# Performance work log

Hardware: AMD Instinct MI355X
Metric: run time of the kernel (lower is better)

Reference implementation:

```python
import jax, jax.numpy as jnp
import numpy as np

HEAD_SIZE = 64
INPUT_SIZE = 1024
B, T = 8, 2048


def setup_inputs() -> dict:
    key = jax.random.key(0)
    kx, kq, kk, kv = jax.random.split(key, 4)
    x = jax.random.normal(kx, (B, T, INPUT_SIZE), dtype=jnp.float32)
    s = 1.0 / np.sqrt(INPUT_SIZE)
    Wq = jax.random.uniform(kq, (INPUT_SIZE, HEAD_SIZE), minval=-s, maxval=s, dtype=jnp.float32)
    Wk = jax.random.uniform(kk, (INPUT_SIZE, HEAD_SIZE), minval=-s, maxval=s, dtype=jnp.float32)
    Wv = jax.random.uniform(kv, (INPUT_SIZE, HEAD_SIZE), minval=-s, maxval=s, dtype=jnp.float32)
    return {"x": x, "Wq": Wq, "Wk": Wk, "Wv": Wv}


def reference(x, Wq, Wk, Wv):
    # Faithful to the torch module: scores = K @ Q^T (note: keys times queries^T),
    # causal mask on upper triangle of that matrix, softmax over last axis,
    # dropout treated as identity (eval), then scores @ V.
    q = jnp.einsum('bti,ih->bth', x, Wq)  # [B,T,H]
    k = jnp.einsum('bti,ih->bth', x, Wk)
    v = jnp.einsum('bti,ih->bth', x, Wv)
    scale = HEAD_SIZE ** -0.5
    scores = jnp.einsum('bth,bsh->bts', k, q) * scale  # [B,T,T] = K Q^T
    Tlen = x.shape[1]
    causal = jnp.tril(jnp.ones((Tlen, Tlen), dtype=bool))
    scores = jnp.where(causal, scores, -jnp.inf)
    w = jax.nn.softmax(scores, axis=-1)
    out = jnp.einsum('bts,bsh->bth', w, v)  # [B,T,H]
    return out
```

## Files before the change

kernel.cpp:

```cpp
#include <hip/hip_runtime.h>

typedef __bf16 bf16_t;
typedef bf16_t bf16x8 __attribute__((ext_vector_type(8)));
typedef float f32x4 __attribute__((ext_vector_type(4)));

#define NB 8
#define TT 2048
#define DIN 1024
#define HH 64
#define MM (NB * TT)

#define CHUNK 4
#define BPB 144
#define NSLOT (NB * BPB)

__device__ __forceinline__ unsigned short f2bf(float f) {
    unsigned int u = __float_as_uint(f);
    u += 0x7fffu + ((u >> 16) & 1u);
    return (unsigned short)(u >> 16);
}

__device__ __forceinline__ void async16(void* l, const void* g) {
    __builtin_amdgcn_global_load_lds(
        (const __attribute__((address_space(1))) unsigned int*)g,
        (__attribute__((address_space(3))) unsigned int*)l, 16, 0, 0);
}

__device__ __forceinline__ int block_detect_f32(const unsigned int* __restrict__ xw,
                                                int tid, int* sflag) {
    if (tid < 64) {
        unsigned int u = xw[tid];
        unsigned int e = (u >> 7) & 0xFFu;
        unsigned long long m = __ballot(e >= 100u && e <= 150u);
        if (tid == 0) *sflag = (__popcll(m) < 48) ? 1 : 0;
    }
    __syncthreads();
    return *sflag;
}

__global__ __launch_bounds__(256) void transpose_w_kernel(
    const void* __restrict__ Wq, const void* __restrict__ Wk,
    const void* __restrict__ Wv, const unsigned int* __restrict__ xw,
    unsigned short* __restrict__ Wt) {
    __shared__ int sflag;
    __shared__ unsigned short ts[64][68];
    const int tid = threadIdx.x;
    const int isf32 = block_detect_f32(xw, tid, &sflag);
    const int w = blockIdx.x >> 4, kt = blockIdx.x & 15;
    const void* W = (w == 0) ? Wq : (w == 1) ? Wk : Wv;
    const int kk = tid >> 4, nn = (tid & 15) * 4;
#pragma unroll
    for (int j = 0; j < 4; ++j) {
        int k = kk + j * 16;
        if (isf32) {
            float4 f = *(const float4*)((const float*)W + (size_t)(kt * 64 + k) * 64 + nn);
            ts[k][nn + 0] = f2bf(f.x); ts[k][nn + 1] = f2bf(f.y);
            ts[k][nn + 2] = f2bf(f.z); ts[k][nn + 3] = f2bf(f.w);
        } else {
            *(uint2*)&ts[k][nn] =
                *(const uint2*)((const unsigned short*)W + (size_t)(kt * 64 + k) * 64 + nn);
        }
    }
    __syncthreads();
    const int n = tid >> 2, k0 = (tid & 3) * 16;
    unsigned short tmp[16];
#pragma unroll
    for (int j = 0; j < 16; ++j) tmp[j] = ts[k0 + j][n];
    unsigned short* dst = Wt + (size_t)(w * 64 + n) * 1024 + kt * 64 + k0;
    *(uint4*)(dst + 0) = *(uint4*)&tmp[0];
    *(uint4*)(dst + 8) = *(uint4*)&tmp[8];
}

#define PN 48

__global__ __launch_bounds__(256, 2) void proj_kernel(
    const void* __restrict__ xraw, const unsigned short* __restrict__ Wt,
    unsigned short* __restrict__ qbuf, unsigned short* __restrict__ kbuf,
    unsigned short* __restrict__ vtbuf) {
    __shared__ int sflag;
    __shared__ __align__(16) unsigned char xsb[64 * 128];
    __shared__ __align__(16) unsigned char wldsb[PN * 128];

    const int tid = threadIdx.x;
    const int isf32 = block_detect_f32((const unsigned int*)xraw, tid, &sflag);
    const int m0 = blockIdx.x * 64;
    const int nh = blockIdx.y;
    const int wave = tid >> 6, lane = tid & 63, quad = lane >> 4, l15 = lane & 15;

    const float* xf = (const float*)xraw;
    const unsigned short* xb = (const unsigned short*)xraw;
    const unsigned char* wg = (const unsigned char*)Wt;

    const unsigned char* wsrc[2];
    unsigned int wdst[2];
    int nw = 0;
#pragma unroll
    for (int j = 0; j < 2; ++j) {
        int c = tid + 256 * j;
        if (c < PN * 8) {
            int R = c >> 3, cc = c & 7;
            int g = cc ^ (R & 7);
            wsrc[nw] = wg + (size_t)(nh * PN + R) * 2048 + g * 16;
            wdst[nw] = c * 16;
            ++nw;
        }
    }

    const int xr = tid >> 2, xc = (tid & 3) * 16;
    const unsigned int xb0 = (unsigned int)(((xc >> 3) ^ (xr & 7)) * 16);
    const unsigned int xb1 = (unsigned int)((((xc >> 3) + 1) ^ (xr & 7)) * 16);
    float4 px[4];
    uint4  pxb[2];
    auto ldx = [&](int k0) {
        if (isf32) {
            const float* g = xf + (size_t)(m0 + xr) * DIN + k0 + xc;
#pragma unroll
            for (int j = 0; j < 4; ++j) px[j] = *(const float4*)(g + j * 4);
        } else {
            const unsigned short* g = xb + (size_t)(m0 + xr) * DIN + k0 + xc;
            pxb[0] = *(const uint4*)(g + 0);
            pxb[1] = *(const uint4*)(g + 8);
        }
    };

    f32x4 acc[3];
#pragma unroll
    for (int ct = 0; ct < 3; ++ct) acc[ct] = (f32x4){0.f, 0.f, 0.f, 0.f};

    ldx(0);
    size_t woff = 0;
    for (int it = 0; it < 16; ++it) {
        __syncthreads();
        {
            unsigned char* xrow = xsb + xr * 128;
            if (isf32) {
                unsigned short t[16];
#pragma unroll
                for (int j = 0; j < 4; ++j) {
                    t[j * 4 + 0] = f2bf(px[j].x); t[j * 4 + 1] = f2bf(px[j].y);
                    t[j * 4 + 2] = f2bf(px[j].z); t[j * 4 + 3] = f2bf(px[j].w);
                }
                *(uint4*)(xrow + xb0) = *(uint4*)&t[0];
                *(uint4*)(xrow + xb1) = *(uint4*)&t[8];
            } else {
                *(uint4*)(xrow + xb0) = pxb[0];
                *(uint4*)(xrow + xb1) = pxb[1];
            }
        }
        for (int j = 0; j < nw; ++j) async16(&wldsb[wdst[j]], wsrc[j] + woff);
        woff += 128;
        __syncthreads();

        if (it < 15) ldx((it + 1) * 64);

#pragma unroll
        for (int ks = 0; ks < 2; ++ks) {
            const int arow = wave * 16 + l15;
            bf16x8 a = *(const bf16x8*)
                (xsb + arow * 128 + (((ks * 4 + quad) ^ (arow & 7)) * 16));
            bf16x8 b[3];
#pragma unroll
            for (int ct = 0; ct < 3; ++ct) {
                const int ri = ct * 16 + l15;
                b[ct] = *(const bf16x8*)
                    (wldsb + ri * 128 + (((ks * 4 + quad) ^ (ri & 7)) * 16));
            }
#pragma unroll
            for (int ct = 0; ct < 3; ++ct)
                acc[ct] = __builtin_amdgcn_mfma_f32_16x16x32_bf16(
                    a, b[ct], acc[ct], 0, 0, 0);
        }
    }

#pragma unroll
    for (int ct = 0; ct < 3; ++ct) {
        int n = nh * PN + ct * 16 + l15;
        int wsel = n >> 6, nn = n & 63;
#pragma unroll
        for (int reg = 0; reg < 4; ++reg) {
            int m = m0 + wave * 16 + quad * 4 + reg;
            unsigned short bv = f2bf(acc[ct][reg]);
            if (wsel == 0)      qbuf[(size_t)m * HH + nn] = bv;
            else if (wsel == 1) kbuf[(size_t)m * HH + nn] = bv;
            else {
                int bb = m >> 11, t = m & 2047;
                vtbuf[((size_t)bb * HH + nn) * TT + t] = bv;
            }
        }
    }
}

__global__ __launch_bounds__(256, 4) void attn_kernel(
    const unsigned short* __restrict__ rowbuf,
    const unsigned short* __restrict__ colbuf,
    const unsigned short* __restrict__ vtbuf,
    float* __restrict__ O_part,
    float* __restrict__ l_part) {

    __shared__ __align__(16) unsigned char Qb[64 * 128];
    __shared__ __align__(16) unsigned char Kb[64 * 128];
    __shared__ __align__(16) unsigned char Vb[64 * 128];
    __shared__ __align__(16) unsigned char Pb[4][16 * 128];

    const int tid  = threadIdx.x;
    const int bid  = blockIdx.x;
    const int b    = bid & 7;
    const int bx   = bid >> 3;
    int rt = 0, ch = 0;
    {
        int a = 0;
        for (int r = 0; r < 32; ++r) {
            int nc = (r + CHUNK) >> 2;
            if (bx < a + nc) { rt = r; ch = bx - a; break; }
            a += nc;
        }
    }
    const int nct = min(CHUNK, rt + 1 - ch * CHUNK);
    const int t0 = rt * 64;
    const int slot = b * BPB + bx;

    const int wave = tid >> 6, lane = tid & 63, quad = lane >> 4, l15 = lane & 15;
    const int sr = tid >> 2, sc = (tid & 3) * 16;
    const unsigned int sb0 = (unsigned int)(((sc >> 3) ^ (sr & 7)) * 16);
    const unsigned int sb1 = (unsigned int)((((sc >> 3) + 1) ^ (sr & 7)) * 16);

    {
        const uint4* g = (const uint4*)(rowbuf + ((size_t)b * TT + t0 + sr) * HH + sc);
        unsigned char* qrow = Qb + sr * 128;
        *(uint4*)(qrow + sb0) = g[0];
        *(uint4*)(qrow + sb1) = g[1];
    }

    f32x4 o[4];
#pragma unroll
    for (int c = 0; c < 4; ++c) o[c] = (f32x4){0.f, 0.f, 0.f, 0.f};
    float ls[4] = {0.f, 0.f, 0.f, 0.f};

    const float SCL2 = 0.125f * 1.4426950408889634f;

    uint4 pk0, pk1, pv0, pv1;
    auto loadKV = [&](int i) {
        const int s0 = (ch * CHUNK + i) * 64;
        const uint4* gk = (const uint4*)(colbuf + ((size_t)b * TT + s0 + sr) * HH + sc);
        pk0 = gk[0]; pk1 = gk[1];
        const uint4* gv = (const uint4*)(vtbuf + ((size_t)b * HH + sr) * TT + s0 + sc);
        pv0 = gv[0]; pv1 = gv[1];
    };
    loadKV(0);

    for (int i = 0; i < nct; ++i) {
        const int stc = ch * CHUNK + i;
        const int s0 = stc * 64;
        {
            unsigned char* krow = Kb + sr * 128;
            unsigned char* vrow = Vb + sr * 128;
            *(uint4*)(krow + sb0) = pk0;
            *(uint4*)(krow + sb1) = pk1;
            *(uint4*)(vrow + sb0) = pv0;
            *(uint4*)(vrow + sb1) = pv1;
        }
        __syncthreads();

        f32x4 scf[4];
#pragma unroll
        for (int c = 0; c < 4; ++c) scf[c] = (f32x4){0.f, 0.f, 0.f, 0.f};
        __builtin_amdgcn_s_setprio(1);
#pragma unroll
        for (int ks = 0; ks < 2; ++ks) {
            const int arow = wave * 16 + l15;
            bf16x8 a = *(const bf16x8*)
                (Qb + arow * 128 + (((ks * 4 + quad) ^ (arow & 7)) * 16));
#pragma unroll
            for (int c = 0; c < 4; ++c) {
                const int ri = c * 16 + l15;
                bf16x8 bb = *(const bf16x8*)
                    (Kb + ri * 128 + (((ks * 4 + quad) ^ (ri & 7)) * 16));
                scf[c] = __builtin_amdgcn_mfma_f32_16x16x32_bf16(a, bb, scf[c], 0, 0, 0);
            }
        }
        __builtin_amdgcn_s_setprio(0);

        if (i + 1 < nct) loadKV(i + 1);

        const bool diag = (stc == rt);
#pragma unroll
        for (int r = 0; r < 4; ++r) {
            const int tg = t0 + wave * 16 + quad * 4 + r;
            const int rr = quad * 4 + r;
            unsigned char* prow = Pb[wave] + rr * 128;
#pragma unroll
            for (int c = 0; c < 4; ++c) {
                float arg = fmaf(scf[c][r], SCL2, -30.f);
                if (diag && (s0 + c * 16 + l15) > tg) arg = -200.f;
                float p = __builtin_amdgcn_exp2f(arg);
                const int cc2 = c * 16 + l15;
                *(unsigned short*)(prow + (((cc2 >> 3) ^ (rr & 7)) * 16)
                                        + (cc2 & 7) * 2) = f2bf(p);
                ls[r] += p;
            }
        }
        __builtin_amdgcn_s_setprio(1);
#pragma unroll
        for (int ks = 0; ks < 2; ++ks) {
            bf16x8 ap = *(const bf16x8*)
                (Pb[wave] + l15 * 128 + (((ks * 4 + quad) ^ (l15 & 7)) * 16));
#pragma unroll
            for (int c = 0; c < 4; ++c) {
                const int ri = c * 16 + l15;
                bf16x8 bv = *(const bf16x8*)
                    (Vb + ri * 128 + (((ks * 4 + quad) ^ (ri & 7)) * 16));
                o[c] = __builtin_amdgcn_mfma_f32_16x16x32_bf16(ap, bv, o[c], 0, 0, 0);
            }
        }
        __builtin_amdgcn_s_setprio(0);
        __syncthreads();
    }

#pragma unroll
    for (int r = 0; r < 4; ++r) {
#pragma unroll
        for (int off = 1; off < 16; off <<= 1) ls[r] += __shfl_xor(ls[r], off);
    }
    if (l15 == 0) {
#pragma unroll
        for (int r = 0; r < 4; ++r)
            l_part[(size_t)slot * 64 + wave * 16 + quad * 4 + r] = ls[r];
    }
#pragma unroll
    for (int c = 0; c < 4; ++c)
#pragma unroll
        for (int r = 0; r < 4; ++r)
            O_part[(size_t)slot * 4096 + (wave * 16 + quad * 4 + r) * 64 + c * 16 + l15] = o[c][r];
}

__global__ __launch_bounds__(256) void combine_kernel(
    const float* __restrict__ O_part, const float* __restrict__ l_part,
    const unsigned int* __restrict__ xw, void* __restrict__ outraw) {
    __shared__ int sflag;
    const int tid = threadIdx.x;
    const int isf32 = block_detect_f32(xw, tid, &sflag);
    const int bid = blockIdx.x;
    const int b = bid & 7;
    const int rg = bid >> 3;
    const int rt = rg >> 2, qr = rg & 3;
    const int nch = (rt + CHUNK) >> 2;
    int off = 0;
    for (int r = 0; r < rt; ++r) off += (r + CHUNK) >> 2;
    const int slot0 = b * BPB + off;

    const int row = qr * 16 + (tid >> 4);
    const int cb = (tid & 15) * 4;
    f32x4 a = (f32x4){0.f, 0.f, 0.f, 0.f};
    float l = 0.f;
    for (int j = 0; j < nch; ++j) {
        a += *(const f32x4*)(O_part + (size_t)(slot0 + j) * 4096 + row * 64 + cb);
        l += l_part[(size_t)(slot0 + j) * 64 + row];
    }
    const float inv = 1.f / l;
    const size_t base = ((size_t)b * TT + rt * 64 + row) * HH + cb;
    if (isf32) {
        f32x4 v = a * inv;
        *(f32x4*)((float*)outraw + base) = v;
    } else {
        unsigned short h[4];
#pragma unroll
        for (int e = 0; e < 4; ++e) h[e] = f2bf(a[e] * inv);
        *(uint2*)((unsigned short*)outraw + base) = *(uint2*)&h[0];
    }
}

extern "C" void kernel_launch(void* const* d_in, const int* in_sizes, int n_in,
                              void* d_out, int out_size, void* d_ws, size_t ws_size,
                              hipStream_t stream) {
    const void* x  = d_in[0];
    const void* Wq = d_in[1];
    const void* Wk = d_in[2];
    const void* Wv = d_in[3];
    unsigned short* ws = (unsigned short*)d_ws;

    unsigned short* qbuf  = ws;
    unsigned short* kbuf  = ws + (size_t)MM * HH;
    unsigned short* vtbuf = ws + (size_t)2 * MM * HH;
    unsigned short* wtbuf = ws + (size_t)3 * MM * HH;
    float* O_part = (float*)(ws + (size_t)3 * MM * HH + 3 * 65536);
    float* l_part = O_part + (size_t)NSLOT * 4096;

    hipLaunchKernelGGL(transpose_w_kernel, dim3(48), dim3(256), 0, stream,
                       Wq, Wk, Wv, (const unsigned int*)x, wtbuf);
    hipLaunchKernelGGL(proj_kernel, dim3(256, 4), dim3(256), 0, stream,
                       x, wtbuf, qbuf, kbuf, vtbuf);
    hipLaunchKernelGGL(attn_kernel, dim3(NSLOT), dim3(256), 0, stream,
                       kbuf, qbuf, vtbuf, O_part, l_part);
    hipLaunchKernelGGL(combine_kernel, dim3(1024), dim3(256), 0, stream,
                       O_part, l_part, (const unsigned int*)x, d_out);
}
```

Baseline: 143.5 us.

## Load projection operands directly from global into MFMA registers, dropping LDS staging

The projection kernel no longer stages x and W tiles through shared memory with barriers. Each lane now loads its MFMA fragments straight from global memory into registers, double-buffered across k-iterations, and the occupancy hint rises from 2 to 4 blocks per CU. This removes the LDS writes and reads, the swizzling and the __syncthreads per iteration. In exchange each wave re-reads the W fragments from global/L2 with less coalesced 16-byte-per-lane accesses, and fp32-to-bf16 conversion now uses the compiler cast instead of the manual rounding helper.

```diff
diff --git a/kernel.cpp b/kernel.cpp
--- a/kernel.cpp
+++ b/kernel.cpp
@@ -18,12 +18,6 @@
     unsigned int u = __float_as_uint(f);
     u += 0x7fffu + ((u >> 16) & 1u);
     return (unsigned short)(u >> 16);
-}
-
-__device__ __forceinline__ void async16(void* l, const void* g) {
-    __builtin_amdgcn_global_load_lds(
-        (const __attribute__((address_space(1))) unsigned int*)g,
-        (__attribute__((address_space(3))) unsigned int*)l, 16, 0, 0);
 }
 
 __device__ __forceinline__ int block_detect_f32(const unsigned int* __restrict__ xw,
@@ -73,102 +67,103 @@
 
 #define PN 48
 
-__global__ __launch_bounds__(256, 2) void proj_kernel(
+__global__ __launch_bounds__(256, 4) void proj_kernel(
     const void* __restrict__ xraw, const unsigned short* __restrict__ Wt,
     unsigned short* __restrict__ qbuf, unsigned short* __restrict__ kbuf,
     unsigned short* __restrict__ vtbuf) {
     __shared__ int sflag;
-    __shared__ __align__(16) unsigned char xsb[64 * 128];
-    __shared__ __align__(16) unsigned char wldsb[PN * 128];
-
     const int tid = threadIdx.x;
     const int isf32 = block_detect_f32((const unsigned int*)xraw, tid, &sflag);
     const int m0 = blockIdx.x * 64;
     const int nh = blockIdx.y;
     const int wave = tid >> 6, lane = tid & 63, quad = lane >> 4, l15 = lane & 15;
 
-    const float* xf = (const float*)xraw;
-    const unsigned short* xb = (const unsigned short*)xraw;
+    const int arow = m0 + wave * 16 + l15;
+    const float* xrowf = (const float*)xraw + (size_t)arow * DIN + quad * 8;
+    const unsigned short* xrowb = (const unsigned short*)xraw + (size_t)arow * DIN + quad * 8;
+
     const unsigned char* wg = (const unsigned char*)Wt;
-
-    const unsigned char* wsrc[2];
-    unsigned int wdst[2];
-    int nw = 0;
-#pragma unroll
-    for (int j = 0; j < 2; ++j) {
-        int c = tid + 256 * j;
-        if (c < PN * 8) {
-            int R = c >> 3, cc = c & 7;
-            int g = cc ^ (R & 7);
-            wsrc[nw] = wg + (size_t)(nh * PN + R) * 2048 + g * 16;
-            wdst[nw] = c * 16;
-            ++nw;
-        }
-    }
-
-    const int xr = tid >> 2, xc = (tid & 3) * 16;
-    const unsigned int xb0 = (unsigned int)(((xc >> 3) ^ (xr & 7)) * 16);
-    const unsigned int xb1 = (unsigned int)((((xc >> 3) + 1) ^ (xr & 7)) * 16);
-    float4 px[4];
-    uint4  pxb[2];
-    auto ldx = [&](int k0) {
-        if (isf32) {
-            const float* g = xf + (size_t)(m0 + xr) * DIN + k0 + xc;
-#pragma unroll
-            for (int j = 0; j < 4; ++j) px[j] = *(const float4*)(g + j * 4);
-        } else {
-            const unsigned short* g = xb + (size_t)(m0 + xr) * DIN + k0 + xc;
-            pxb[0] = *(const uint4*)(g + 0);
-            pxb[1] = *(const uint4*)(g + 8);
+    const unsigned char* wp0 = wg + (size_t)(nh * PN +  0 + l15) * 2048 + quad * 16;
+    const unsigned char* wp1 = wg + (size_t)(nh * PN + 16 + l15) * 2048 + quad * 16;
+    const unsigned char* wp2 = wg + (size_t)(nh * PN + 32 + l15) * 2048 + quad * 16;
+
+    f32x4 acc[3];
+#pragma unroll
+    for (int ct = 0; ct < 3; ++ct) acc[ct] = (f32x4){0.f, 0.f, 0.f, 0.f};
+
+    auto loadw = [&](int it, uint4 (&w)[6]) {
+        const size_t o = (size_t)it * 128;
+#pragma unroll
+        for (int ks = 0; ks < 2; ++ks) {
+            w[0 * 2 + ks] = *(const uint4*)(wp0 + o + ks * 64);
+            w[1 * 2 + ks] = *(const uint4*)(wp1 + o + ks * 64);
+            w[2 * 2 + ks] = *(const uint4*)(wp2 + o + ks * 64);
         }
     };
-
-    f32x4 acc[3];
-#pragma unroll
-    for (int ct = 0; ct < 3; ++ct) acc[ct] = (f32x4){0.f, 0.f, 0.f, 0.f};
-
-    ldx(0);
-    size_t woff = 0;
-    for (int it = 0; it < 16; ++it) {
-        __syncthreads();
-        {
-            unsigned char* xrow = xsb + xr * 128;
-            if (isf32) {
-                unsigned short t[16];
-#pragma unroll
-                for (int j = 0; j < 4; ++j) {
-                    t[j * 4 + 0] = f2bf(px[j].x); t[j * 4 + 1] = f2bf(px[j].y);
-                    t[j * 4 + 2] = f2bf(px[j].z); t[j * 4 + 3] = f2bf(px[j].w);
-                }
-                *(uint4*)(xrow + xb0) = *(uint4*)&t[0];
-                *(uint4*)(xrow + xb1) = *(uint4*)&t[8];
-            } else {
-                *(uint4*)(xrow + xb0) = pxb[0];
-                *(uint4*)(xrow + xb1) = pxb[1];
-            }
-        }
-        for (int j = 0; j < nw; ++j) async16(&wldsb[wdst[j]], wsrc[j] + woff);
-        woff += 128;
-        __syncthreads();
-
-        if (it < 15) ldx((it + 1) * 64);
-
-#pragma unroll
-        for (int ks = 0; ks < 2; ++ks) {
-            const int arow = wave * 16 + l15;
-            bf16x8 a = *(const bf16x8*)
-                (xsb + arow * 128 + (((ks * 4 + quad) ^ (arow & 7)) * 16));
-            bf16x8 b[3];
-#pragma unroll
-            for (int ct = 0; ct < 3; ++ct) {
-                const int ri = ct * 16 + l15;
-                b[ct] = *(const bf16x8*)
-                    (wldsb + ri * 128 + (((ks * 4 + quad) ^ (ri & 7)) * 16));
-            }
-#pragma unroll
-            for (int ct = 0; ct < 3; ++ct)
-                acc[ct] = __builtin_amdgcn_mfma_f32_16x16x32_bf16(
-                    a, b[ct], acc[ct], 0, 0, 0);
+    auto wfrag = [](const uint4& u) -> bf16x8 {
+        union { uint4 u; bf16x8 b; } c; c.u = u; return c.b;
+    };
+
+    if (isf32) {
+        auto loadx = [&](int it, float4 (&x)[4]) {
+            const float* p = xrowf + it * 64;
+#pragma unroll
+            for (int ks = 0; ks < 2; ++ks) {
+                x[ks * 2 + 0] = *(const float4*)(p + ks * 32);
+                x[ks * 2 + 1] = *(const float4*)(p + ks * 32 + 4);
+            }
+        };
+        auto mk = [](const float4& f0, const float4& f1) -> bf16x8 {
+            bf16x8 a;
+            a[0] = (bf16_t)f0.x; a[1] = (bf16_t)f0.y;
+            a[2] = (bf16_t)f0.z; a[3] = (bf16_t)f0.w;
+            a[4] = (bf16_t)f1.x; a[5] = (bf16_t)f1.y;
+            a[6] = (bf16_t)f1.z; a[7] = (bf16_t)f1.w;
+            return a;
+        };
+        auto compute = [&](float4 (&x)[4], uint4 (&w)[6]) {
+#pragma unroll
+            for (int ks = 0; ks < 2; ++ks) {
+                bf16x8 a = mk(x[ks * 2], x[ks * 2 + 1]);
+#pragma unroll
+                for (int ct = 0; ct < 3; ++ct)
+                    acc[ct] = __builtin_amdgcn_mfma_f32_16x16x32_bf16(
+                        a, wfrag(w[ct * 2 + ks]), acc[ct], 0, 0, 0);
+            }
+        };
+        float4 xA[4], xB[4];
+        uint4  wA[6], wB[6];
+        loadx(0, xA); loadw(0, wA);
+        for (int it = 0; it < 16; it += 2) {
+            loadx(it + 1, xB); loadw(it + 1, wB);
+            compute(xA, wA);
+            if (it + 2 < 16) { loadx(it + 2, xA); loadw(it + 2, wA); }
+            compute(xB, wB);
+        }
+    } else {
+        auto loadx = [&](int it, uint4 (&x)[2]) {
+            const unsigned short* p = xrowb + it * 64;
+            x[0] = *(const uint4*)(p + 0 * 32);
+            x[1] = *(const uint4*)(p + 1 * 32);
+        };
+        auto compute = [&](uint4 (&x)[2], uint4 (&w)[6]) {
+#pragma unroll
+            for (int ks = 0; ks < 2; ++ks) {
+                bf16x8 a = wfrag(x[ks]);
+#pragma unroll
+                for (int ct = 0; ct < 3; ++ct)
+                    acc[ct] = __builtin_amdgcn_mfma_f32_16x16x32_bf16(
+                        a, wfrag(w[ct * 2 + ks]), acc[ct], 0, 0, 0);
+            }
+        };
+        uint4 xA[2], xB[2];
+        uint4 wA[6], wB[6];
+        loadx(0, xA); loadw(0, wA);
+        for (int it = 0; it < 16; it += 2) {
+            loadx(it + 1, xB); loadw(it + 1, wB);
+            compute(xA, wA);
+            if (it + 2 < 16) { loadx(it + 2, xA); loadw(it + 2, wA); }
+            compute(xB, wB);
         }
     }
 
```

Result: slower. 186.7 us (+30.1%).

## Halve projection barriers with double-wide W stage; keep Q fragments in registers

Applied to the files above, without the earlier changes.

The projection kernel now loads two 64-wide K slices of W per barrier pair into a doubled LDS buffer and runs two compute steps between syncs. This halves the number of __syncthreads per block, at the cost of extra LDS use. Separately, the attention kernel drops the Q shared-memory tile and loads each wave's Q MFMA operands straight from global memory into registers. That removes LDS traffic and LDS footprint, in exchange for more registers and an uncoalesced Q load.

```diff
diff --git a/kernel.cpp b/kernel.cpp
--- a/kernel.cpp
+++ b/kernel.cpp
@@ -79,7 +79,7 @@
     unsigned short* __restrict__ vtbuf) {
     __shared__ int sflag;
     __shared__ __align__(16) unsigned char xsb[64 * 128];
-    __shared__ __align__(16) unsigned char wldsb[PN * 128];
+    __shared__ __align__(16) unsigned char wldsb[2 * PN * 128];
 
     const int tid = threadIdx.x;
     const int isf32 = block_detect_f32((const unsigned int*)xraw, tid, &sflag);
@@ -91,19 +91,16 @@
     const unsigned short* xb = (const unsigned short*)xraw;
     const unsigned char* wg = (const unsigned char*)Wt;
 
-    const unsigned char* wsrc[2];
-    unsigned int wdst[2];
-    int nw = 0;
-#pragma unroll
-    for (int j = 0; j < 2; ++j) {
-        int c = tid + 256 * j;
-        if (c < PN * 8) {
-            int R = c >> 3, cc = c & 7;
-            int g = cc ^ (R & 7);
-            wsrc[nw] = wg + (size_t)(nh * PN + R) * 2048 + g * 16;
-            wdst[nw] = c * 16;
-            ++nw;
-        }
+    const unsigned char* wsrc[3];
+    unsigned int wdst[3];
+#pragma unroll
+    for (int j = 0; j < 3; ++j) {
+        int c2 = tid + 256 * j;
+        int p = (c2 >= PN * 8) ? 1 : 0;
+        int c = c2 - p * (PN * 8);
+        int R = c >> 3, cc = c & 7;
+        wsrc[j] = wg + (size_t)(nh * PN + R) * 2048 + ((cc ^ (R & 7)) * 16) + p * 128;
+        wdst[j] = (unsigned int)c2 * 16;
     }
 
     const int xr = tid >> 2, xc = (tid & 3) * 16;
@@ -122,37 +119,29 @@
             pxb[1] = *(const uint4*)(g + 8);
         }
     };
+    auto writeXs = [&]() {
+        unsigned char* xrow = xsb + xr * 128;
+        if (isf32) {
+            unsigned short t[16];
+#pragma unroll
+            for (int j = 0; j < 4; ++j) {
+                t[j * 4 + 0] = f2bf(px[j].x); t[j * 4 + 1] = f2bf(px[j].y);
+                t[j * 4 + 2] = f2bf(px[j].z); t[j * 4 + 3] = f2bf(px[j].w);
+            }
+            *(uint4*)(xrow + xb0) = *(uint4*)&t[0];
+            *(uint4*)(xrow + xb1) = *(uint4*)&t[8];
+        } else {
+            *(uint4*)(xrow + xb0) = pxb[0];
+            *(uint4*)(xrow + xb1) = pxb[1];
+        }
+    };
 
     f32x4 acc[3];
 #pragma unroll
     for (int ct = 0; ct < 3; ++ct) acc[ct] = (f32x4){0.f, 0.f, 0.f, 0.f};
 
-    ldx(0);
-    size_t woff = 0;
-    for (int it = 0; it < 16; ++it) {
-        __syncthreads();
-        {
-            unsigned char* xrow = xsb + xr * 128;
-            if (isf32) {
-                unsigned short t[16];
-#pragma unroll
-                for (int j = 0; j < 4; ++j) {
-                    t[j * 4 + 0] = f2bf(px[j].x); t[j * 4 + 1] = f2bf(px[j].y);
-                    t[j * 4 + 2] = f2bf(px[j].z); t[j * 4 + 3] = f2bf(px[j].w);
-                }
-                *(uint4*)(xrow + xb0) = *(uint4*)&t[0];
-                *(uint4*)(xrow + xb1) = *(uint4*)&t[8];
-            } else {
-                *(uint4*)(xrow + xb0) = pxb[0];
-                *(uint4*)(xrow + xb1) = pxb[1];
-            }
-        }
-        for (int j = 0; j < nw; ++j) async16(&wldsb[wdst[j]], wsrc[j] + woff);
-        woff += 128;
-        __syncthreads();
-
-        if (it < 15) ldx((it + 1) * 64);
-
+    auto compute = [&](int p) {
+        const unsigned char* wb = wldsb + p * (PN * 128);
 #pragma unroll
         for (int ks = 0; ks < 2; ++ks) {
             const int arow = wave * 16 + l15;
@@ -163,13 +152,26 @@
             for (int ct = 0; ct < 3; ++ct) {
                 const int ri = ct * 16 + l15;
                 b[ct] = *(const bf16x8*)
-                    (wldsb + ri * 128 + (((ks * 4 + quad) ^ (ri & 7)) * 16));
+                    (wb + ri * 128 + (((ks * 4 + quad) ^ (ri & 7)) * 16));
             }
 #pragma unroll
             for (int ct = 0; ct < 3; ++ct)
                 acc[ct] = __builtin_amdgcn_mfma_f32_16x16x32_bf16(
                     a, b[ct], acc[ct], 0, 0, 0);
         }
+    };
+
+    ldx(0);
+    for (int g = 0; g < 8; ++g) {
+        __syncthreads();
+        for (int j = 0; j < 3; ++j) async16(&wldsb[wdst[j]], wsrc[j] + g * 256);
+        writeXs();
+        __syncthreads();
+        ldx(2 * g * 64 + 64);
+        compute(0);
+        writeXs();
+        if (g < 7) ldx(2 * g * 64 + 128);
+        compute(1);
     }
 
 #pragma unroll
@@ -197,7 +199,6 @@
     float* __restrict__ O_part,
     float* __restrict__ l_part) {
 
-    __shared__ __align__(16) unsigned char Qb[64 * 128];
     __shared__ __align__(16) unsigned char Kb[64 * 128];
     __shared__ __align__(16) unsigned char Vb[64 * 128];
     __shared__ __align__(16) unsigned char Pb[4][16 * 128];
@@ -224,11 +225,12 @@
     const unsigned int sb0 = (unsigned int)(((sc >> 3) ^ (sr & 7)) * 16);
     const unsigned int sb1 = (unsigned int)((((sc >> 3) + 1) ^ (sr & 7)) * 16);
 
+    bf16x8 aq[2];
     {
-        const uint4* g = (const uint4*)(rowbuf + ((size_t)b * TT + t0 + sr) * HH + sc);
-        unsigned char* qrow = Qb + sr * 128;
-        *(uint4*)(qrow + sb0) = g[0];
-        *(uint4*)(qrow + sb1) = g[1];
+        const unsigned short* qp =
+            rowbuf + ((size_t)b * TT + t0 + wave * 16 + l15) * HH + quad * 8;
+        aq[0] = *(const bf16x8*)(qp);
+        aq[1] = *(const bf16x8*)(qp + 32);
     }
 
     f32x4 o[4];
@@ -267,15 +269,12 @@
         __builtin_amdgcn_s_setprio(1);
 #pragma unroll
         for (int ks = 0; ks < 2; ++ks) {
-            const int arow = wave * 16 + l15;
-            bf16x8 a = *(const bf16x8*)
-                (Qb + arow * 128 + (((ks * 4 + quad) ^ (arow & 7)) * 16));
 #pragma unroll
             for (int c = 0; c < 4; ++c) {
                 const int ri = c * 16 + l15;
                 bf16x8 bb = *(const bf16x8*)
                     (Kb + ri * 128 + (((ks * 4 + quad) ^ (ri & 7)) * 16));
-                scf[c] = __builtin_amdgcn_mfma_f32_16x16x32_bf16(a, bb, scf[c], 0, 0, 0);
+                scf[c] = __builtin_amdgcn_mfma_f32_16x16x32_bf16(aq[ks], bb, scf[c], 0, 0, 0);
             }
         }
         __builtin_amdgcn_s_setprio(0);
```

After: 142.3 us, median of 2. About the same (-0.8%).
